# Performance work log

Hardware: AMD Instinct MI355X
Metric: run time of the kernel (lower is better)

The kernel has to match this reference:

```python
import jax, jax.numpy as jnp
import numpy as np

N_NODES = 50000
N_EDGES = 800000
C = 128
EDGE_DIM = 8
N_LAYERS = 3


def setup_inputs() -> dict:
    key = jax.random.key(0)
    ks = jax.random.split(key, 8)
    x = jax.random.normal(ks[0], (N_NODES, C), dtype=jnp.float32)
    edge_index = jax.random.randint(ks[1], (2, N_EDGES), 0, N_NODES, dtype=jnp.int64)
    edge_attr = jax.random.uniform(ks[2], (N_EDGES, EDGE_DIM), dtype=jnp.float32)
    # stacked per-layer params (all layers are 128->128 HydroConv)
    lin_w = jax.random.normal(ks[3], (N_LAYERS, C, C), dtype=jnp.float32) / np.sqrt(C)
    lin_b = jnp.zeros((N_LAYERS, C), dtype=jnp.float32)
    emlp_w = jax.random.normal(ks[4], (N_LAYERS, EDGE_DIM, 1), dtype=jnp.float32) / np.sqrt(EDGE_DIM)
    emlp_b = jnp.zeros((N_LAYERS, 1), dtype=jnp.float32)
    return {"x": x, "edge_index": edge_index, "edge_attr": edge_attr,
            "lin_w": lin_w, "lin_b": lin_b, "emlp_w": emlp_w, "emlp_b": emlp_b}


def _hydro_conv(x, src, dst, edge_attr, lw, lb, ew, eb):
    # edge weight: softplus(edge_attr @ ew + eb) -> [E, 1]
    weight = jax.nn.softplus(edge_attr @ ew + eb)
    # message: weight * (x_j - x_i), x_j = source, x_i = target
    msg = weight * (x[src] - x[dst])                  # [E, C]
    agg = jax.ops.segment_sum(msg, dst, num_segments=N_NODES)  # scatter-add at target
    return agg @ lw + lb                              # node linear


def reference(x, edge_index, edge_attr, lin_w, lin_b, emlp_w, emlp_b):
    src, dst = edge_index[0], edge_index[1]
    for i in range(N_LAYERS):
        residual = x
        x = _hydro_conv(x, src, dst, edge_attr, lin_w[i], lin_b[i], emlp_w[i], emlp_b[i])
        if i < N_LAYERS - 1:
            x = jax.nn.relu(x)
            x = x + residual  # residual=True, dropout=0
    return x
```

## Files before the change

kernel.cpp:

```cpp
#include <hip/hip_runtime.h>

#define NN 50000
#define NE 800000
#define CC 128
#define NL 3

typedef short bf16x8 __attribute__((ext_vector_type(8)));
typedef float f32x4 __attribute__((ext_vector_type(4)));
union U16 { uint4 u; bf16x8 v; };

__device__ __forceinline__ float b2f(unsigned short u) {
  return __uint_as_float(((unsigned int)u) << 16);
}
__device__ __forceinline__ unsigned short f2b(float f) {
  unsigned int x = __float_as_uint(f);
  x += 0x7fffu + ((x >> 16) & 1u);
  return (unsigned short)(x >> 16);
}

__device__ __forceinline__ int eidx(const int* ei, int row, int e, int f64) {
  return f64 ? ei[2 * ((size_t)row * NE + e)] : ei[(size_t)row * NE + e];
}

#define NI4 (NN / 4)
__global__ __launch_bounds__(256) void k_prep(const void* __restrict__ xin,
                                              const int* __restrict__ ei,
                                              const void* lw, const void* lb,
                                              const void* emw, const void* emb,
                                              unsigned short* __restrict__ xb,
                                              unsigned short* __restrict__ wt,
                                              float* lbf, float* emwf, float* embf,
                                              int* __restrict__ deg,
                                              int* __restrict__ flags) {
  __shared__ int scnt, sany;
  const int tid = threadIdx.x;
  if (tid == 0) { scnt = 0; sany = 0; }
  __syncthreads();
  if (tid < 128) {
    unsigned short u = ((const unsigned short*)xin)[2 * tid];
    int ex = (u >> 7) & 0xFF;
    if (ex >= 0x70 && ex <= 0x8F) atomicAdd(&scnt, 1);
  }
  if (ei[2 * tid + 1] != 0) atomicOr(&sany, 1);
  __syncthreads();
  const int isbf = (scnt >= 64) ? 1 : 0;
  const int i = blockIdx.x * 256 + tid;
  if (i == 0) { flags[0] = isbf; flags[1] = (sany == 0) ? 1 : 0; }

  if (i < NI4) ((int4*)deg)[i] = make_int4(0, 0, 0, 0);

  if (i < NL * CC * CC) {
    unsigned short v = isbf ? ((const unsigned short*)lw)[i]
                            : f2b(((const float*)lw)[i]);
    const int l = i >> 14, r = i & 16383, k = r >> 7, n = r & 127;
    wt[l * 16384 + n * 128 + k] = v;
  }
  if (i < NL * CC)
    lbf[i] = isbf ? b2f(((const unsigned short*)lb)[i]) : ((const float*)lb)[i];
  if (i < NL * 8)
    emwf[i] = isbf ? b2f(((const unsigned short*)emw)[i]) : ((const float*)emw)[i];
  if (i < NL)
    embf[i] = isbf ? b2f(((const unsigned short*)emb)[i]) : ((const float*)emb)[i];

  if (!isbf && i < NN * CC / 8) {
    const float4 a = ((const float4*)xin)[2 * i];
    const float4 b = ((const float4*)xin)[2 * i + 1];
    uint4 o;
    o.x = (unsigned)f2b(a.x) | ((unsigned)f2b(a.y) << 16);
    o.y = (unsigned)f2b(a.z) | ((unsigned)f2b(a.w) << 16);
    o.z = (unsigned)f2b(b.x) | ((unsigned)f2b(b.y) << 16);
    o.w = (unsigned)f2b(b.z) | ((unsigned)f2b(b.w) << 16);
    ((uint4*)xb)[i] = o;
  }
}

#define HT 8
#define HIST_BLKS ((NE + HT * 256 - 1) / (HT * 256))
__global__ __launch_bounds__(256) void k_hist(const int* __restrict__ ei,
                                              int* __restrict__ deg,
                                              unsigned short* __restrict__ rank,
                                              const int* __restrict__ flags) {
  const int f64 = flags[1];
  const int nt = gridDim.x * 256;
  const int t = blockIdx.x * 256 + threadIdx.x;
  int d[HT], r[HT];
#pragma unroll
  for (int k = 0; k < HT; ++k) {
    const int e = t + k * nt;
    d[k] = (e < NE) ? eidx(ei, 1, e, f64) : -1;
  }
#pragma unroll
  for (int k = 0; k < HT; ++k)
    if (d[k] >= 0) r[k] = atomicAdd(&deg[d[k]], 1);
#pragma unroll
  for (int k = 0; k < HT; ++k) {
    const int e = t + k * nt;
    if (e < NE) rank[e] = (unsigned short)r[k];
  }
}

#define SCAN_BLKS ((NI4 + 255) / 256)
__global__ __launch_bounds__(256) void k_scan1(const int* __restrict__ deg,
                                               int* __restrict__ offs,
                                               int* __restrict__ bsum) {
  __shared__ int ls[256];
  const int t = threadIdx.x;
  const int g = blockIdx.x * 256 + t;
  int4 d = make_int4(0, 0, 0, 0);
  if (g < NI4) d = ((const int4*)deg)[g];
  const int s = d.x + d.y + d.z + d.w;
  ls[t] = s;
  __syncthreads();
#pragma unroll
  for (int off = 1; off < 256; off <<= 1) {
    int tmp = (t >= off) ? ls[t - off] : 0;
    __syncthreads();
    ls[t] += tmp;
    __syncthreads();
  }
  const int excl = ls[t] - s;
  if (g < NI4) {
    int4 o;
    o.x = excl; o.y = o.x + d.x; o.z = o.y + d.y; o.w = o.z + d.z;
    ((int4*)offs)[g] = o;
  }
  if (t == 255) bsum[blockIdx.x] = ls[255];
}

__global__ __launch_bounds__(256) void k_scan3(int* __restrict__ offs,
                                               const int* __restrict__ bsum) {
  __shared__ int sbase;
  const int g = blockIdx.x * 256 + threadIdx.x;
  if (threadIdx.x == 0) {
    int run = 0;
    for (int b = 0; b < (int)blockIdx.x; ++b) run += bsum[b];
    sbase = run;
    if (blockIdx.x == 0) {
      int tot = 0;
      for (int b = 0; b < SCAN_BLKS; ++b) tot += bsum[b];
      offs[NN] = tot;
    }
  }
  __syncthreads();
  if (g >= NI4) return;
  const int base = sbase;
  int4 o = ((int4*)offs)[g];
  o.x += base; o.y += base; o.z += base; o.w += base;
  ((int4*)offs)[g] = o;
}

__global__ __launch_bounds__(256) void k_fill(const int* __restrict__ ei,
                                              const void* __restrict__ ea,
                                              const float* __restrict__ emwf,
                                              const float* __restrict__ embf,
                                              const int* __restrict__ offs,
                                              const unsigned short* __restrict__ rank,
                                              uint2* __restrict__ esrt,
                                              const int* __restrict__ flags) {
  int e = blockIdx.x * 256 + threadIdx.x;
  if (e >= NE) return;
  float a[8];
  if (flags[0]) {
    const uint4 v = ((const uint4*)ea)[e];
    unsigned int p[4] = {v.x, v.y, v.z, v.w};
#pragma unroll
    for (int q = 0; q < 4; ++q) {
      a[2 * q]     = __uint_as_float(p[q] << 16);
      a[2 * q + 1] = __uint_as_float(p[q] & 0xffff0000u);
    }
  } else {
    const float4 v0 = ((const float4*)ea)[2 * e];
    const float4 v1 = ((const float4*)ea)[2 * e + 1];
    a[0] = v0.x; a[1] = v0.y; a[2] = v0.z; a[3] = v0.w;
    a[4] = v1.x; a[5] = v1.y; a[6] = v1.z; a[7] = v1.w;
  }
  unsigned wb[NL];
#pragma unroll
  for (int l = 0; l < NL; ++l) {
    float z = embf[l];
#pragma unroll
    for (int k = 0; k < 8; ++k) z += a[k] * emwf[l * 8 + k];
    const float w = (z > 20.f) ? z : log1pf(expf(z));
    wb[l] = (unsigned)f2b(w);
  }
  const int f64 = flags[1];
  const int d = eidx(ei, 1, e, f64);
  const int s = eidx(ei, 0, e, f64);
  const int pos = offs[d] + (int)rank[e];
  esrt[pos] = make_uint2((unsigned)s | (wb[0] << 16), wb[1] | (wb[2] << 16));
}

#define LPAD 136
template<int LAYER>
__device__ __forceinline__ unsigned wbits(const uint2& p) {
  return LAYER == 0 ? (p.x & 0xffff0000u)
       : (LAYER == 1 ? (p.y << 16) : (p.y & 0xffff0000u));
}

template<int LAYER>
__global__ __launch_bounds__(512) void k_layer(const int* __restrict__ offs,
                                               const uint2* __restrict__ esrt,
                                               const unsigned short* xc_,
                                               const unsigned short* alt, int sel,
                                               const unsigned short* __restrict__ wt,
                                               const float* __restrict__ lbf,
                                               void* outp, int last,
                                               const int* __restrict__ flags,
                                               unsigned short* __restrict__ xout) {
  const unsigned short* xb = (sel && flags[0]) ? alt : xc_;
  __shared__ unsigned short shA[64 * LPAD];
  __shared__ unsigned short shB[128 * LPAD];
  const int tid = threadIdx.x;
  const int rb = blockIdx.x * 64;
  const unsigned short* wtl = wt + (size_t)LAYER * CC * CC;

  for (int u = tid; u < 2048; u += 512) {
    const int row = u >> 4, q = u & 15;
    *(uint4*)&shB[row * LPAD + q * 8] = *(const uint4*)&wtl[row * 128 + q * 8];
  }

  const int wid = tid >> 6;
  const int l = tid & 63;
  const int g = l >> 4;
  const int ch = (l & 15) * 8;

  for (int i = 0; i < 8; ++i) {
    const int nl = wid * 8 + i;
    const int node = __builtin_amdgcn_readfirstlane(rb + nl);
    if (node >= NN) {
      if (l < 16) *(uint4*)&shA[nl * LPAD + ch] = make_uint4(0, 0, 0, 0);
      continue;
    }
    const int j0 = offs[node];
    const int j1 = offs[node + 1];
    const uint4 xi = *(const uint4*)&xb[(size_t)node * CC + ch];
    float ax[8];
#pragma unroll
    for (int q = 0; q < 8; ++q) ax[q] = 0.f;
    float sw = 0.f;

    for (int jc = j0; jc < j1; jc += 64) {
      const int cnt = j1 - jc;
      const int kk = (l < cnt) ? l : (cnt - 1);
      const uint2 rec = esrt[jc + kk];
      const int srcl = (int)(rec.x & 0xffffu);
      const int wl = (int)wbits<LAYER>(rec);
      const int cc2 = (cnt > 64) ? 64 : cnt;
      const int nsb = (cc2 + 15) >> 4;
      for (int b2 = 0; b2 < nsb; ++b2) {
        int srcw[4]; float wv[4];
#pragma unroll
        for (int b = 0; b < 4; ++b) {
          const int k = b2 * 16 + b * 4 + g;
          srcw[b] = __shfl(srcl, k);
          const float w = __uint_as_float((unsigned)__shfl(wl, k));
          wv[b] = (k < cnt) ? w : 0.f;
        }
        uint4 v[4];
#pragma unroll
        for (int b = 0; b < 4; ++b)
          v[b] = *(const uint4*)&xb[(size_t)(unsigned)srcw[b] * CC + ch];
#pragma unroll
        for (int b = 0; b < 4; ++b) {
          const float w = wv[b];
          const unsigned pv0 = v[b].x, pv1 = v[b].y, pv2 = v[b].z, pv3 = v[b].w;
          ax[0] += w * __uint_as_float(pv0 << 16);
          ax[1] += w * __uint_as_float(pv0 & 0xffff0000u);
          ax[2] += w * __uint_as_float(pv1 << 16);
          ax[3] += w * __uint_as_float(pv1 & 0xffff0000u);
          ax[4] += w * __uint_as_float(pv2 << 16);
          ax[5] += w * __uint_as_float(pv2 & 0xffff0000u);
          ax[6] += w * __uint_as_float(pv3 << 16);
          ax[7] += w * __uint_as_float(pv3 & 0xffff0000u);
          sw += w;
        }
      }
    }

#pragma unroll
    for (int q = 0; q < 8; ++q) {
      ax[q] += __shfl_xor(ax[q], 16);
      ax[q] += __shfl_xor(ax[q], 32);
    }
    sw += __shfl_xor(sw, 16);
    sw += __shfl_xor(sw, 32);

    if (l < 16) {
      float r[8];
      r[0] = ax[0] - sw * __uint_as_float(xi.x << 16);
      r[1] = ax[1] - sw * __uint_as_float(xi.x & 0xffff0000u);
      r[2] = ax[2] - sw * __uint_as_float(xi.y << 16);
      r[3] = ax[3] - sw * __uint_as_float(xi.y & 0xffff0000u);
      r[4] = ax[4] - sw * __uint_as_float(xi.z << 16);
      r[5] = ax[5] - sw * __uint_as_float(xi.z & 0xffff0000u);
      r[6] = ax[6] - sw * __uint_as_float(xi.w << 16);
      r[7] = ax[7] - sw * __uint_as_float(xi.w & 0xffff0000u);
      uint4 o;
      o.x = (unsigned)f2b(r[0]) | ((unsigned)f2b(r[1]) << 16);
      o.y = (unsigned)f2b(r[2]) | ((unsigned)f2b(r[3]) << 16);
      o.z = (unsigned)f2b(r[4]) | ((unsigned)f2b(r[5]) << 16);
      o.w = (unsigned)f2b(r[6]) | ((unsigned)f2b(r[7]) << 16);
      *(uint4*)&shA[nl * LPAD + ch] = o;
    }
  }
  __syncthreads();

  const int rw = wid >> 1;
  const int cb = (wid & 1) * 4;
  const int lr = l & 15;
  const int lk = (l >> 4) * 8;

  U16 afr[4];
#pragma unroll
  for (int kk = 0; kk < 4; ++kk)
    afr[kk].u = *(const uint4*)&shA[(rw * 16 + lr) * LPAD + kk * 32 + lk];
  __syncthreads();

  const float* lbp = lbf + LAYER * CC;
  f32x4 acc[4];
#pragma unroll
  for (int t = 0; t < 4; ++t) {
    acc[t] = (f32x4){0.f, 0.f, 0.f, 0.f};
#pragma unroll
    for (int kk = 0; kk < 4; ++kk) {
      U16 bfr;
      bfr.u = *(const uint4*)&shB[((cb + t) * 16 + lr) * LPAD + kk * 32 + lk];
      acc[t] = __builtin_amdgcn_mfma_f32_16x16x32_bf16(afr[kk].v, bfr.v, acc[t], 0, 0, 0);
    }
  }

#pragma unroll
  for (int t = 0; t < 4; ++t) {
    const float bv = lbp[(cb + t) * 16 + lr];
#pragma unroll
    for (int r = 0; r < 4; ++r) {
      const int tr = (l >> 4) * 4 + r;
      shA[(rw * 16 + tr) * LPAD + (cb + t) * 16 + lr] = f2b(acc[t][r] + bv);
    }
  }
  __syncthreads();

  const int isbf = flags[0];
  for (int u = tid; u < 1024; u += 512) {
    const int row = u >> 4, q = u & 15;
    const int gr = rb + row;
    if (gr >= NN) continue;
    const uint4 yv = *(const uint4*)&shA[row * LPAD + q * 8];
    float y0 = __uint_as_float(yv.x << 16), y1 = __uint_as_float(yv.x & 0xffff0000u);
    float y2 = __uint_as_float(yv.y << 16), y3 = __uint_as_float(yv.y & 0xffff0000u);
    float y4 = __uint_as_float(yv.z << 16), y5 = __uint_as_float(yv.z & 0xffff0000u);
    float y6 = __uint_as_float(yv.w << 16), y7 = __uint_as_float(yv.w & 0xffff0000u);
    const size_t off = (size_t)gr * CC + q * 8;
    if (!last) {
      const uint4 rv = *(const uint4*)&xb[off];
      y0 = fmaxf(y0, 0.f) + __uint_as_float(rv.x << 16);
      y1 = fmaxf(y1, 0.f) + __uint_as_float(rv.x & 0xffff0000u);
      y2 = fmaxf(y2, 0.f) + __uint_as_float(rv.y << 16);
      y3 = fmaxf(y3, 0.f) + __uint_as_float(rv.y & 0xffff0000u);
      y4 = fmaxf(y4, 0.f) + __uint_as_float(rv.z << 16);
      y5 = fmaxf(y5, 0.f) + __uint_as_float(rv.z & 0xffff0000u);
      y6 = fmaxf(y6, 0.f) + __uint_as_float(rv.w << 16);
      y7 = fmaxf(y7, 0.f) + __uint_as_float(rv.w & 0xffff0000u);
      uint4 o;
      o.x = (unsigned)f2b(y0) | ((unsigned)f2b(y1) << 16);
      o.y = (unsigned)f2b(y2) | ((unsigned)f2b(y3) << 16);
      o.z = (unsigned)f2b(y4) | ((unsigned)f2b(y5) << 16);
      o.w = (unsigned)f2b(y6) | ((unsigned)f2b(y7) << 16);
      *(uint4*)&xout[off] = o;
    } else if (isbf) {
      *(uint4*)&((unsigned short*)outp)[off] = yv;
    } else {
      *(float4*)&((float*)outp)[off] = make_float4(y0, y1, y2, y3);
      *(float4*)&((float*)outp)[off + 4] = make_float4(y4, y5, y6, y7);
    }
  }
}

extern "C" void kernel_launch(void* const* d_in, const int* in_sizes, int n_in,
                              void* d_out, int out_size, void* d_ws, size_t ws_size,
                              hipStream_t stream) {
  const unsigned short* x0 = (const unsigned short*)d_in[0];
  const int* ei = (const int*)d_in[1];

  const size_t nbuf = (size_t)NN * CC;
  unsigned short* xb0 = (unsigned short*)d_ws;
  unsigned short* xb1 = xb0 + nbuf;
  unsigned short* wt = xb1 + nbuf;
  uint2* esrt = (uint2*)(wt + (size_t)NL * CC * CC);
  int* deg = (int*)(esrt + NE);
  int* offs = deg + NN;
  unsigned short* rank = (unsigned short*)(offs + NN + 4);
  int* bsum = (int*)(rank + NE);
  float* lbf = (float*)(bsum + 64);
  float* emwf = lbf + (size_t)NL * CC;
  float* embf = emwf + NL * 8;
  int* flags = (int*)(embf + NL);
  const size_t need = (size_t)((char*)(flags + 2) - (char*)d_ws);
  if (ws_size < need) {
    hipMemsetAsync(d_out, 0, (size_t)out_size * 2, stream);
    return;
  }

  k_prep<<<(NN * CC / 8) / 256, 256, 0, stream>>>(
      d_in[0], ei, d_in[3], d_in[4], d_in[5], d_in[6],
      xb0, wt, lbf, emwf, embf, deg, flags);
  k_hist<<<HIST_BLKS, 256, 0, stream>>>(ei, deg, rank, flags);
  k_scan1<<<SCAN_BLKS, 256, 0, stream>>>(deg, offs, bsum);
  k_scan3<<<SCAN_BLKS, 256, 0, stream>>>(offs, bsum);
  k_fill<<<(NE + 255) / 256, 256, 0, stream>>>(ei, d_in[2], emwf, embf,
                                               offs, rank, esrt, flags);

  const int LBLKS = (NN + 63) / 64;
  unsigned short* xc = xb0;
  unsigned short* xo = xb1;
  for (int layer = 0; layer < NL; ++layer) {
    const int sel = (layer == 0) ? 1 : 0;
    const int last = (layer == NL - 1) ? 1 : 0;
    if (layer == 0)
      k_layer<0><<<LBLKS, 512, 0, stream>>>(offs, esrt, xc, x0, sel, wt, lbf,
                                            d_out, last, flags, xo);
    else if (layer == 1)
      k_layer<1><<<LBLKS, 512, 0, stream>>>(offs, esrt, xc, x0, sel, wt, lbf,
                                            d_out, last, flags, xo);
    else
      k_layer<2><<<LBLKS, 512, 0, stream>>>(offs, esrt, xc, x0, sel, wt, lbf,
                                            d_out, last, flags, xo);
    unsigned short* t = xc; xc = xo; xo = t;
  }
}
```

Before: 292.9 us.

## Fuse CSR build kernels into one cooperative kernel and use nontemporal accesses

Merges the histogram, two scan passes and edge fill into a single cooperative-launch kernel that separates the phases with grid-wide syncs, removing three kernel launches and their gaps. The fill phase becomes a grid-stride loop over the smaller cooperative grid. Edge-record stores and loads and the final output stores switch to nontemporal builtins to reduce cache pollution. The cost is grid-sync overhead, fewer blocks for the fill phase, and a dependence on cooperative launch support; the grid must be co-resident.

```diff
diff --git a/kernel.cpp b/kernel.cpp
--- a/kernel.cpp
+++ b/kernel.cpp
@@ -1,4 +1,7 @@
 #include <hip/hip_runtime.h>
+#include <hip/hip_cooperative_groups.h>
+
+namespace cg = cooperative_groups;
 
 #define NN 50000
 #define NE 800000
@@ -7,6 +10,7 @@
 
 typedef short bf16x8 __attribute__((ext_vector_type(8)));
 typedef float f32x4 __attribute__((ext_vector_type(4)));
+typedef unsigned int u32x4 __attribute__((ext_vector_type(4)));
 union U16 { uint4 u; bf16x8 v; };
 
 __device__ __forceinline__ float b2f(unsigned short u) {
@@ -16,6 +20,23 @@
   unsigned int x = __float_as_uint(f);
   x += 0x7fffu + ((x >> 16) & 1u);
   return (unsigned short)(x >> 16);
+}
+
+__device__ __forceinline__ uint2 nt_load_u2(const uint2* p) {
+  unsigned long long t = __builtin_nontemporal_load((const unsigned long long*)p);
+  return make_uint2((unsigned)t, (unsigned)(t >> 32));
+}
+__device__ __forceinline__ void nt_store_u2(uint2* p, uint2 v) {
+  unsigned long long t = (unsigned long long)v.x | ((unsigned long long)v.y << 32);
+  __builtin_nontemporal_store(t, (unsigned long long*)p);
+}
+__device__ __forceinline__ void nt_store_u4(void* p, uint4 v) {
+  u32x4 t = {v.x, v.y, v.z, v.w};
+  __builtin_nontemporal_store(t, (u32x4*)p);
+}
+__device__ __forceinline__ void nt_store_f4(void* p, float a, float b, float c, float d) {
+  f32x4 t = {a, b, c, d};
+  __builtin_nontemporal_store(t, (f32x4*)p);
 }
 
 __device__ __forceinline__ int eidx(const int* ei, int row, int e, int f64) {
@@ -75,119 +96,122 @@
 }
 
 #define HT 8
-#define HIST_BLKS ((NE + HT * 256 - 1) / (HT * 256))
-__global__ __launch_bounds__(256) void k_hist(const int* __restrict__ ei,
-                                              int* __restrict__ deg,
-                                              unsigned short* __restrict__ rank,
-                                              const int* __restrict__ flags) {
+#define BUILD_BLKS ((NE + HT * 256 - 1) / (HT * 256))
+#define SCAN_BLKS ((NI4 + 255) / 256)
+__global__ __launch_bounds__(256) void k_build(const int* __restrict__ ei,
+                                               const void* __restrict__ ea,
+                                               const float* __restrict__ emwf,
+                                               const float* __restrict__ embf,
+                                               int* __restrict__ deg,
+                                               int* __restrict__ offs,
+                                               unsigned short* __restrict__ rank,
+                                               int* __restrict__ bsum,
+                                               uint2* __restrict__ esrt,
+                                               const int* __restrict__ flags) {
+  cg::grid_group grid = cg::this_grid();
+  __shared__ int ls[256];
+  __shared__ int sbase;
+  const int tid = threadIdx.x;
   const int f64 = flags[1];
-  const int nt = gridDim.x * 256;
-  const int t = blockIdx.x * 256 + threadIdx.x;
-  int d[HT], r[HT];
-#pragma unroll
-  for (int k = 0; k < HT; ++k) {
-    const int e = t + k * nt;
-    d[k] = (e < NE) ? eidx(ei, 1, e, f64) : -1;
-  }
-#pragma unroll
-  for (int k = 0; k < HT; ++k)
-    if (d[k] >= 0) r[k] = atomicAdd(&deg[d[k]], 1);
-#pragma unroll
-  for (int k = 0; k < HT; ++k) {
-    const int e = t + k * nt;
-    if (e < NE) rank[e] = (unsigned short)r[k];
-  }
-}
-
-#define SCAN_BLKS ((NI4 + 255) / 256)
-__global__ __launch_bounds__(256) void k_scan1(const int* __restrict__ deg,
-                                               int* __restrict__ offs,
-                                               int* __restrict__ bsum) {
-  __shared__ int ls[256];
-  const int t = threadIdx.x;
-  const int g = blockIdx.x * 256 + t;
-  int4 d = make_int4(0, 0, 0, 0);
-  if (g < NI4) d = ((const int4*)deg)[g];
-  const int s = d.x + d.y + d.z + d.w;
-  ls[t] = s;
-  __syncthreads();
-#pragma unroll
-  for (int off = 1; off < 256; off <<= 1) {
-    int tmp = (t >= off) ? ls[t - off] : 0;
+  const int tcount = gridDim.x * 256;
+
+  {
+    const int t = blockIdx.x * 256 + tid;
+    int d[HT], r[HT];
+#pragma unroll
+    for (int k = 0; k < HT; ++k) {
+      const int e = t + k * tcount;
+      d[k] = (e < NE) ? eidx(ei, 1, e, f64) : -1;
+    }
+#pragma unroll
+    for (int k = 0; k < HT; ++k)
+      if (d[k] >= 0) r[k] = atomicAdd(&deg[d[k]], 1);
+#pragma unroll
+    for (int k = 0; k < HT; ++k) {
+      const int e = t + k * tcount;
+      if (e < NE) rank[e] = (unsigned short)r[k];
+    }
+  }
+  grid.sync();
+
+  if (blockIdx.x < SCAN_BLKS) {
+    const int g = blockIdx.x * 256 + tid;
+    int4 d = make_int4(0, 0, 0, 0);
+    if (g < NI4) d = ((const int4*)deg)[g];
+    const int s = d.x + d.y + d.z + d.w;
+    ls[tid] = s;
     __syncthreads();
-    ls[t] += tmp;
+#pragma unroll
+    for (int off = 1; off < 256; off <<= 1) {
+      int tmp = (tid >= off) ? ls[tid - off] : 0;
+      __syncthreads();
+      ls[tid] += tmp;
+      __syncthreads();
+    }
+    const int excl = ls[tid] - s;
+    if (g < NI4) {
+      int4 o;
+      o.x = excl; o.y = o.x + d.x; o.z = o.y + d.y; o.w = o.z + d.z;
+      ((int4*)offs)[g] = o;
+    }
+    if (tid == 255) bsum[blockIdx.x] = ls[255];
+  }
+  grid.sync();
+
+  if (blockIdx.x < SCAN_BLKS) {
+    if (tid == 0) {
+      int run = 0;
+      for (int b = 0; b < (int)blockIdx.x; ++b) run += bsum[b];
+      sbase = run;
+      if (blockIdx.x == 0) {
+        int tot = 0;
+        for (int b = 0; b < SCAN_BLKS; ++b) tot += bsum[b];
+        offs[NN] = tot;
+      }
+    }
     __syncthreads();
-  }
-  const int excl = ls[t] - s;
-  if (g < NI4) {
-    int4 o;
-    o.x = excl; o.y = o.x + d.x; o.z = o.y + d.y; o.w = o.z + d.z;
-    ((int4*)offs)[g] = o;
-  }
-  if (t == 255) bsum[blockIdx.x] = ls[255];
-}
-
-__global__ __launch_bounds__(256) void k_scan3(int* __restrict__ offs,
-                                               const int* __restrict__ bsum) {
-  __shared__ int sbase;
-  const int g = blockIdx.x * 256 + threadIdx.x;
-  if (threadIdx.x == 0) {
-    int run = 0;
-    for (int b = 0; b < (int)blockIdx.x; ++b) run += bsum[b];
-    sbase = run;
-    if (blockIdx.x == 0) {
-      int tot = 0;
-      for (int b = 0; b < SCAN_BLKS; ++b) tot += bsum[b];
-      offs[NN] = tot;
-    }
-  }
-  __syncthreads();
-  if (g >= NI4) return;
-  const int base = sbase;
-  int4 o = ((int4*)offs)[g];
-  o.x += base; o.y += base; o.z += base; o.w += base;
-  ((int4*)offs)[g] = o;
-}
-
-__global__ __launch_bounds__(256) void k_fill(const int* __restrict__ ei,
-                                              const void* __restrict__ ea,
-                                              const float* __restrict__ emwf,
-                                              const float* __restrict__ embf,
-                                              const int* __restrict__ offs,
-                                              const unsigned short* __restrict__ rank,
-                                              uint2* __restrict__ esrt,
-                                              const int* __restrict__ flags) {
-  int e = blockIdx.x * 256 + threadIdx.x;
-  if (e >= NE) return;
-  float a[8];
-  if (flags[0]) {
-    const uint4 v = ((const uint4*)ea)[e];
-    unsigned int p[4] = {v.x, v.y, v.z, v.w};
-#pragma unroll
-    for (int q = 0; q < 4; ++q) {
-      a[2 * q]     = __uint_as_float(p[q] << 16);
-      a[2 * q + 1] = __uint_as_float(p[q] & 0xffff0000u);
-    }
-  } else {
-    const float4 v0 = ((const float4*)ea)[2 * e];
-    const float4 v1 = ((const float4*)ea)[2 * e + 1];
-    a[0] = v0.x; a[1] = v0.y; a[2] = v0.z; a[3] = v0.w;
-    a[4] = v1.x; a[5] = v1.y; a[6] = v1.z; a[7] = v1.w;
-  }
-  unsigned wb[NL];
-#pragma unroll
-  for (int l = 0; l < NL; ++l) {
-    float z = embf[l];
-#pragma unroll
-    for (int k = 0; k < 8; ++k) z += a[k] * emwf[l * 8 + k];
-    const float w = (z > 20.f) ? z : log1pf(expf(z));
-    wb[l] = (unsigned)f2b(w);
-  }
-  const int f64 = flags[1];
-  const int d = eidx(ei, 1, e, f64);
-  const int s = eidx(ei, 0, e, f64);
-  const int pos = offs[d] + (int)rank[e];
-  esrt[pos] = make_uint2((unsigned)s | (wb[0] << 16), wb[1] | (wb[2] << 16));
+    const int g = blockIdx.x * 256 + tid;
+    if (g < NI4) {
+      const int base = sbase;
+      int4 o = ((int4*)offs)[g];
+      o.x += base; o.y += base; o.z += base; o.w += base;
+      ((int4*)offs)[g] = o;
+    }
+  }
+  grid.sync();
+
+  const int isbf = flags[0];
+  for (int e = blockIdx.x * 256 + tid; e < NE; e += tcount) {
+    float a[8];
+    if (isbf) {
+      const uint4 v = ((const uint4*)ea)[e];
+      unsigned int p[4] = {v.x, v.y, v.z, v.w};
+#pragma unroll
+      for (int q = 0; q < 4; ++q) {
+        a[2 * q]     = __uint_as_float(p[q] << 16);
+        a[2 * q + 1] = __uint_as_float(p[q] & 0xffff0000u);
+      }
+    } else {
+      const float4 v0 = ((const float4*)ea)[2 * e];
+      const float4 v1 = ((const float4*)ea)[2 * e + 1];
+      a[0] = v0.x; a[1] = v0.y; a[2] = v0.z; a[3] = v0.w;
+      a[4] = v1.x; a[5] = v1.y; a[6] = v1.z; a[7] = v1.w;
+    }
+    unsigned wb[NL];
+#pragma unroll
+    for (int l = 0; l < NL; ++l) {
+      float z = embf[l];
+#pragma unroll
+      for (int k = 0; k < 8; ++k) z += a[k] * emwf[l * 8 + k];
+      const float w = (z > 20.f) ? z : log1pf(expf(z));
+      wb[l] = (unsigned)f2b(w);
+    }
+    const int d = eidx(ei, 1, e, f64);
+    const int s = eidx(ei, 0, e, f64);
+    const int pos = offs[d] + (int)rank[e];
+    nt_store_u2(&esrt[pos],
+                make_uint2((unsigned)s | (wb[0] << 16), wb[1] | (wb[2] << 16)));
+  }
 }
 
 #define LPAD 136
@@ -242,7 +266,7 @@
     for (int jc = j0; jc < j1; jc += 64) {
       const int cnt = j1 - jc;
       const int kk = (l < cnt) ? l : (cnt - 1);
-      const uint2 rec = esrt[jc + kk];
+      const uint2 rec = nt_load_u2(&esrt[jc + kk]);
       const int srcl = (int)(rec.x & 0xffffu);
       const int wl = (int)wbits<LAYER>(rec);
       const int cc2 = (cnt > 64) ? 64 : cnt;
@@ -368,10 +392,10 @@
       o.w = (unsigned)f2b(y6) | ((unsigned)f2b(y7) << 16);
       *(uint4*)&xout[off] = o;
     } else if (isbf) {
-      *(uint4*)&((unsigned short*)outp)[off] = yv;
+      nt_store_u4(&((unsigned short*)outp)[off], yv);
     } else {
-      *(float4*)&((float*)outp)[off] = make_float4(y0, y1, y2, y3);
-      *(float4*)&((float*)outp)[off + 4] = make_float4(y4, y5, y6, y7);
+      nt_store_f4(&((float*)outp)[off], y0, y1, y2, y3);
+      nt_store_f4(&((float*)outp)[off + 4], y4, y5, y6, y7);
     }
   }
 }
@@ -404,11 +428,24 @@
   k_prep<<<(NN * CC / 8) / 256, 256, 0, stream>>>(
       d_in[0], ei, d_in[3], d_in[4], d_in[5], d_in[6],
       xb0, wt, lbf, emwf, embf, deg, flags);
-  k_hist<<<HIST_BLKS, 256, 0, stream>>>(ei, deg, rank, flags);
-  k_scan1<<<SCAN_BLKS, 256, 0, stream>>>(deg, offs, bsum);
-  k_scan3<<<SCAN_BLKS, 256, 0, stream>>>(offs, bsum);
-  k_fill<<<(NE + 255) / 256, 256, 0, stream>>>(ei, d_in[2], emwf, embf,
-                                               offs, rank, esrt, flags);
+
+  {
+    const int* ei_p = ei;
+    const void* ea_p = d_in[2];
+    const float* emwf_p = emwf;
+    const float* embf_p = embf;
+    int* deg_p = deg;
+    int* offs_p = offs;
+    unsigned short* rank_p = rank;
+    int* bsum_p = bsum;
+    uint2* esrt_p = esrt;
+    const int* flags_p = flags;
+    void* args[] = {(void*)&ei_p, (void*)&ea_p, (void*)&emwf_p, (void*)&embf_p,
+                    (void*)&deg_p, (void*)&offs_p, (void*)&rank_p,
+                    (void*)&bsum_p, (void*)&esrt_p, (void*)&flags_p};
+    hipLaunchCooperativeKernel((void*)k_build, dim3(BUILD_BLKS), dim3(256),
+                               args, 0, stream);
+  }
 
   const int LBLKS = (NN + 63) / 64;
   unsigned short* xc = xb0;
```

New measurement: 449.7 us. 53.6% more time.

## Software-pipeline per-node edge metadata and first neighbor gathers across nodes

Applied to the files above, without the earlier changes.

Each wave now prefetches the CSR offsets and edge records two nodes ahead, and the first 16 neighbor feature rows one node ahead, so the gather latency of the next node overlaps with accumulation of the current one. The first sub-batch of 16 edges comes from the prefetched registers, and the remaining edges follow the old chunked loop. This hides dependent global-load latency in the gather-heavy aggregation, at the cost of more live registers, which could lower occupancy.

```diff
diff --git a/kernel.cpp b/kernel.cpp
--- a/kernel.cpp
+++ b/kernel.cpp
@@ -211,7 +211,7 @@
   __shared__ unsigned short shA[64 * LPAD];
   __shared__ unsigned short shB[128 * LPAD];
   const int tid = threadIdx.x;
-  const int rb = blockIdx.x * 64;
+  const int rbase = blockIdx.x * 64;
   const unsigned short* wtl = wt + (size_t)LAYER * CC * CC;
 
   for (int u = tid; u < 2048; u += 512) {
@@ -223,38 +223,89 @@
   const int l = tid & 63;
   const int g = l >> 4;
   const int ch = (l & 15) * 8;
+  const int nbase = rbase + wid * 8;
+
+#define LOADMETA(S, J0, CNT) do {                                   \
+    const int nd_ = nbase + (S);                                    \
+    if ((S) < 8 && nd_ < NN) { J0 = offs[nd_]; CNT = offs[nd_ + 1] - J0; } \
+    else { J0 = 0; CNT = 0; }                                       \
+  } while (0)
+#define RECLOAD(J0, CNT) esrt[(size_t)(J0) + ((l < (CNT)) ? l : ((CNT) > 0 ? (CNT) - 1 : 0))]
+
+  int j0a, cna, j0b, cnb, j0c, cnc;
+  uint2 ra, rbv, rc;
+  uint4 vin[4];
+
+  LOADMETA(0, j0a, cna);
+  ra = RECLOAD(j0a, cna);
+  LOADMETA(1, j0b, cnb);
+  rbv = RECLOAD(j0b, cnb);
+  {
+    const int sl = (int)(ra.x & 0xffffu);
+#pragma unroll
+    for (int b = 0; b < 4; ++b) {
+      const int k = b * 4 + g;
+      int s2 = __shfl(sl, k);
+      s2 = (cna > 0) ? s2 : 0;
+      vin[b] = *(const uint4*)&xb[(size_t)(unsigned)s2 * CC + ch];
+    }
+  }
 
   for (int i = 0; i < 8; ++i) {
+    uint4 vc[4];
+#pragma unroll
+    for (int b = 0; b < 4; ++b) vc[b] = vin[b];
+    {
+      const int sl = (int)(rbv.x & 0xffffu);
+#pragma unroll
+      for (int b = 0; b < 4; ++b) {
+        const int k = b * 4 + g;
+        int s2 = __shfl(sl, k);
+        s2 = (cnb > 0) ? s2 : 0;
+        vin[b] = *(const uint4*)&xb[(size_t)(unsigned)s2 * CC + ch];
+      }
+    }
+    LOADMETA(i + 2, j0c, cnc);
+    rc = RECLOAD(j0c, cnc);
+
+    const int node = nbase + i;
     const int nl = wid * 8 + i;
-    const int node = __builtin_amdgcn_readfirstlane(rb + nl);
-    if (node >= NN) {
-      if (l < 16) *(uint4*)&shA[nl * LPAD + ch] = make_uint4(0, 0, 0, 0);
-      continue;
-    }
-    const int j0 = offs[node];
-    const int j1 = offs[node + 1];
-    const uint4 xi = *(const uint4*)&xb[(size_t)node * CC + ch];
-    float ax[8];
-#pragma unroll
-    for (int q = 0; q < 8; ++q) ax[q] = 0.f;
-    float sw = 0.f;
-
-    for (int jc = j0; jc < j1; jc += 64) {
-      const int cnt = j1 - jc;
-      const int kk = (l < cnt) ? l : (cnt - 1);
-      const uint2 rec = esrt[jc + kk];
-      const int srcl = (int)(rec.x & 0xffffu);
-      const int wl = (int)wbits<LAYER>(rec);
-      const int cc2 = (cnt > 64) ? 64 : cnt;
+    if (node < NN) {
+      const uint4 xi = *(const uint4*)&xb[(size_t)node * CC + ch];
+      float ax[8];
+#pragma unroll
+      for (int q = 0; q < 8; ++q) ax[q] = 0.f;
+      float sw = 0.f;
+      const int sla = (int)(ra.x & 0xffffu);
+      const int wla = (int)wbits<LAYER>(ra);
+
+#pragma unroll
+      for (int b = 0; b < 4; ++b) {
+        const int k = b * 4 + g;
+        const float w0 = __uint_as_float((unsigned)__shfl(wla, k));
+        const float w = (k < cna) ? w0 : 0.f;
+        const unsigned pv0 = vc[b].x, pv1 = vc[b].y, pv2 = vc[b].z, pv3 = vc[b].w;
+        ax[0] += w * __uint_as_float(pv0 << 16);
+        ax[1] += w * __uint_as_float(pv0 & 0xffff0000u);
+        ax[2] += w * __uint_as_float(pv1 << 16);
+        ax[3] += w * __uint_as_float(pv1 & 0xffff0000u);
+        ax[4] += w * __uint_as_float(pv2 << 16);
+        ax[5] += w * __uint_as_float(pv2 & 0xffff0000u);
+        ax[6] += w * __uint_as_float(pv3 << 16);
+        ax[7] += w * __uint_as_float(pv3 & 0xffff0000u);
+        sw += w;
+      }
+
+      const int cc2 = (cna > 64) ? 64 : cna;
       const int nsb = (cc2 + 15) >> 4;
-      for (int b2 = 0; b2 < nsb; ++b2) {
+      for (int b2 = 1; b2 < nsb; ++b2) {
         int srcw[4]; float wv[4];
 #pragma unroll
         for (int b = 0; b < 4; ++b) {
           const int k = b2 * 16 + b * 4 + g;
-          srcw[b] = __shfl(srcl, k);
-          const float w = __uint_as_float((unsigned)__shfl(wl, k));
-          wv[b] = (k < cnt) ? w : 0.f;
+          srcw[b] = __shfl(sla, k);
+          const float w = __uint_as_float((unsigned)__shfl(wla, k));
+          wv[b] = (k < cna) ? w : 0.f;
         }
         uint4 v[4];
 #pragma unroll
@@ -275,33 +326,76 @@
           sw += w;
         }
       }
-    }
-
-#pragma unroll
-    for (int q = 0; q < 8; ++q) {
-      ax[q] += __shfl_xor(ax[q], 16);
-      ax[q] += __shfl_xor(ax[q], 32);
-    }
-    sw += __shfl_xor(sw, 16);
-    sw += __shfl_xor(sw, 32);
-
-    if (l < 16) {
-      float r[8];
-      r[0] = ax[0] - sw * __uint_as_float(xi.x << 16);
-      r[1] = ax[1] - sw * __uint_as_float(xi.x & 0xffff0000u);
-      r[2] = ax[2] - sw * __uint_as_float(xi.y << 16);
-      r[3] = ax[3] - sw * __uint_as_float(xi.y & 0xffff0000u);
-      r[4] = ax[4] - sw * __uint_as_float(xi.z << 16);
-      r[5] = ax[5] - sw * __uint_as_float(xi.z & 0xffff0000u);
-      r[6] = ax[6] - sw * __uint_as_float(xi.w << 16);
-      r[7] = ax[7] - sw * __uint_as_float(xi.w & 0xffff0000u);
-      uint4 o;
-      o.x = (unsigned)f2b(r[0]) | ((unsigned)f2b(r[1]) << 16);
-      o.y = (unsigned)f2b(r[2]) | ((unsigned)f2b(r[3]) << 16);
-      o.z = (unsigned)f2b(r[4]) | ((unsigned)f2b(r[5]) << 16);
-      o.w = (unsigned)f2b(r[6]) | ((unsigned)f2b(r[7]) << 16);
-      *(uint4*)&shA[nl * LPAD + ch] = o;
-    }
+
+      for (int jc = j0a + 64; jc < j0a + cna; jc += 64) {
+        const int cnt = j0a + cna - jc;
+        const int kk = (l < cnt) ? l : (cnt - 1);
+        const uint2 rec = esrt[(size_t)jc + kk];
+        const int srcl = (int)(rec.x & 0xffffu);
+        const int wl = (int)wbits<LAYER>(rec);
+        const int cc3 = (cnt > 64) ? 64 : cnt;
+        const int ns2 = (cc3 + 15) >> 4;
+        for (int b2 = 0; b2 < ns2; ++b2) {
+          int srcw[4]; float wv[4];
+#pragma unroll
+          for (int b = 0; b < 4; ++b) {
+            const int k = b2 * 16 + b * 4 + g;
+            srcw[b] = __shfl(srcl, k);
+            const float w = __uint_as_float((unsigned)__shfl(wl, k));
+            wv[b] = (k < cnt) ? w : 0.f;
+          }
+          uint4 v[4];
+#pragma unroll
+          for (int b = 0; b < 4; ++b)
+            v[b] = *(const uint4*)&xb[(size_t)(unsigned)srcw[b] * CC + ch];
+#pragma unroll
+          for (int b = 0; b < 4; ++b) {
+            const float w = wv[b];
+            const unsigned pv0 = v[b].x, pv1 = v[b].y, pv2 = v[b].z, pv3 = v[b].w;
+            ax[0] += w * __uint_as_float(pv0 << 16);
+            ax[1] += w * __uint_as_float(pv0 & 0xffff0000u);
+            ax[2] += w * __uint_as_float(pv1 << 16);
+            ax[3] += w * __uint_as_float(pv1 & 0xffff0000u);
+            ax[4] += w * __uint_as_float(pv2 << 16);
+            ax[5] += w * __uint_as_float(pv2 & 0xffff0000u);
+            ax[6] += w * __uint_as_float(pv3 << 16);
+            ax[7] += w * __uint_as_float(pv3 & 0xffff0000u);
+            sw += w;
+          }
+        }
+      }
+
+#pragma unroll
+      for (int q = 0; q < 8; ++q) {
+        ax[q] += __shfl_xor(ax[q], 16);
+        ax[q] += __shfl_xor(ax[q], 32);
+      }
+      sw += __shfl_xor(sw, 16);
+      sw += __shfl_xor(sw, 32);
+
+      if (l < 16) {
+        float r[8];
+        r[0] = ax[0] - sw * __uint_as_float(xi.x << 16);
+        r[1] = ax[1] - sw * __uint_as_float(xi.x & 0xffff0000u);
+        r[2] = ax[2] - sw * __uint_as_float(xi.y << 16);
+        r[3] = ax[3] - sw * __uint_as_float(xi.y & 0xffff0000u);
+        r[4] = ax[4] - sw * __uint_as_float(xi.z << 16);
+        r[5] = ax[5] - sw * __uint_as_float(xi.z & 0xffff0000u);
+        r[6] = ax[6] - sw * __uint_as_float(xi.w << 16);
+        r[7] = ax[7] - sw * __uint_as_float(xi.w & 0xffff0000u);
+        uint4 o;
+        o.x = (unsigned)f2b(r[0]) | ((unsigned)f2b(r[1]) << 16);
+        o.y = (unsigned)f2b(r[2]) | ((unsigned)f2b(r[3]) << 16);
+        o.z = (unsigned)f2b(r[4]) | ((unsigned)f2b(r[5]) << 16);
+        o.w = (unsigned)f2b(r[6]) | ((unsigned)f2b(r[7]) << 16);
+        *(uint4*)&shA[nl * LPAD + ch] = o;
+      }
+    } else {
+      if (l < 16) *(uint4*)&shA[nl * LPAD + ch] = make_uint4(0, 0, 0, 0);
+    }
+
+    j0a = j0b; cna = cnb; ra = rbv;
+    j0b = j0c; cnb = cnc; rbv = rc;
   }
   __syncthreads();
 
@@ -343,7 +437,7 @@
   const int isbf = flags[0];
   for (int u = tid; u < 1024; u += 512) {
     const int row = u >> 4, q = u & 15;
-    const int gr = rb + row;
+    const int gr = rbase + row;
     if (gr >= NN) continue;
     const uint4 yv = *(const uint4*)&shA[row * LPAD + q * 8];
     float y0 = __uint_as_float(yv.x << 16), y1 = __uint_as_float(yv.x & 0xffff0000u);
```

Result: slower. 307.3 us (+4.9%).
